# Kernel tuning notes

Measured on AMD Instinct MI355X. Metric: run time of the kernel, lower is better.

The kernel has to match this reference:

```python
import jax, jax.numpy as jnp
import numpy as np

NEG_SLOPE = 0.2  # PyG GATConv default negative_slope


def setup_inputs() -> dict:
    key = jax.random.key(0)
    k_x, k_e, k_w, k_as, k_ad = jax.random.split(key, 5)
    B, F, N, D, E, L = 2, 16, 5000, 128, 40000, 3
    x = jax.random.normal(k_x, (B, F, N, D), dtype=jnp.float32)
    edge_index = jax.random.randint(k_e, (B, F, 2, E), 0, N, dtype=jnp.int64)
    Ws = jax.random.normal(k_w, (L, D, D), dtype=jnp.float32) / np.float32(np.sqrt(D))
    att_src = jax.random.normal(k_as, (L, D), dtype=jnp.float32) / np.float32(np.sqrt(D))
    att_dst = jax.random.normal(k_ad, (L, D), dtype=jnp.float32) / np.float32(np.sqrt(D))
    bias = jnp.zeros((L, D), dtype=jnp.float32)
    return {"x": x, "edge_index": edge_index, "Ws": Ws,
            "att_src": att_src, "att_dst": att_dst, "bias": bias}


def _gat_layer(h, src, dst, n, W, a_s, a_d, b):
    # h: [n, D] node features; src/dst: [E_tot] edge endpoints (self-loops included)
    h2 = h @ W                                   # [n, D] transformed features
    s = h2 @ a_s                                 # [n] per-node source score
    d = h2 @ a_d                                 # [n] per-node dest score
    e = jax.nn.leaky_relu(s[src] + d[dst], NEG_SLOPE)   # [E_tot] raw attention
    m = jax.lax.stop_gradient(jax.ops.segment_max(e, dst, num_segments=n))
    ex = jnp.exp(e - m[dst])                     # numerically stable softmax per dst
    denom = jax.ops.segment_sum(ex, dst, num_segments=n)
    alpha = ex / denom[dst]                      # [E_tot] normalized attention
    out = jax.ops.segment_sum(alpha[:, None] * h2[src], dst, num_segments=n) + b
    return jax.nn.relu(out)


def reference(x, edge_index, Ws, att_src, att_dst, bias):
    B, F, N, D = x.shape
    n = B * F * N
    h = x.reshape(n, D)
    # faithful to torch: (BF,2,E).view(2,-1) is a raw row-major reshape
    ei = edge_index.reshape(2, -1)
    loop = jnp.arange(n, dtype=ei.dtype)         # PyG GATConv adds self-loops
    src = jnp.concatenate([ei[0], loop])
    dst = jnp.concatenate([ei[1], loop])
    for l in range(Ws.shape[0]):                 # fixed small layer loop
        h = _gat_layer(h, src, dst, n, Ws[l], att_src[l], att_dst[l], bias[l])
    return h.reshape(B, F, N, D)
```

## Files before the change

kernel.cpp:

```cpp
#include <hip/hip_runtime.h>
#include <math.h>

#define NODES_TOTAL 160000
#define NODES_REAL  5000
#define D 128
#define NEG 0.2f
#define KP2 128
#define HL2 (128 * KP2)
#define WT2_L (2 * HL2)
#define CHUNK 16384

typedef unsigned short ushort_t;
typedef unsigned int uint_t;
typedef __attribute__((ext_vector_type(8))) __bf16 bf16x8;
typedef __attribute__((ext_vector_type(4))) float f32x4;
union BF8 { bf16x8 v; ushort_t u[8]; };

__device__ __forceinline__ void split2(float x, ushort_t& hi, ushort_t& lo) {
    unsigned u = __float_as_uint(x);
    hi = (ushort_t)(u >> 16);
    float hif = __uint_as_float(u & 0xffff0000u);
    lo = (ushort_t)(__float_as_uint(x - hif) >> 16);
}
__device__ __forceinline__ uint_t encmax(float f) {
    uint_t b = __float_as_uint(f);
    return b ^ ((uint_t)((int)b >> 31) | 0x80000000u);
}
__device__ __forceinline__ float decmax(uint_t u) {
    uint_t b = (u & 0x80000000u) ? (u ^ 0x80000000u) : ~u;
    return __uint_as_float(b);
}

__global__ void wsplit_kernel(const float* __restrict__ Ws, ushort_t* __restrict__ Wm,
                              int* __restrict__ counts, uint_t* __restrict__ gmaxu) {
    int gid = blockIdx.x * 256 + threadIdx.x;
    if (gid < NODES_REAL) counts[gid] = 0;
    if (gid < 3) gmaxu[gid] = 0u;
    int l  = blockIdx.x >> 3;
    int n  = (blockIdx.x & 7) * 16 + (threadIdx.x >> 4);
    int c8 = threadIdx.x & 15;
    int k0 = c8 * 8;
    const float* src = Ws + (size_t)l * D * D;
    union { ushort_t u[8]; uint4 v; } hi, lo;
    #pragma unroll
    for (int j = 0; j < 8; ++j) split2(src[(size_t)(k0 + j) * D + n], hi.u[j], lo.u[j]);
    int ct = n >> 4, m16 = n & 15, kc = c8 >> 2, qq = c8 & 3;
    int lane = qq * 16 + m16;
    ushort_t* d2 = Wm + (size_t)l * WT2_L + ((ct * 4 + kc) * 2 + 0) * 512 + lane * 8;
    *(uint4*)d2 = hi.v;
    *(uint4*)(d2 + 512) = lo.v;
}

__global__ __launch_bounds__(256)
void rank2_kernel(const int* __restrict__ ei, int* __restrict__ counts,
                  int* __restrict__ bases, ushort_t* __restrict__ rank16, int Eh) {
    __shared__ uint_t lc[NODES_REAL];
    int c = blockIdx.x, tid = threadIdx.x;
    for (int i = tid; i < NODES_REAL; i += 256) lc[i] = 0u;
    __syncthreads();
    int e0 = c * CHUNK;
    #pragma unroll 4
    for (int k = 0; k < CHUNK / 256; ++k) {
        int e = e0 + k * 256 + tid;
        if (e < Eh) {
            int d = ei[Eh + e];
            uint_t r = atomicAdd(&lc[d], 1u);
            rank16[e] = (ushort_t)r;
        }
    }
    __syncthreads();
    for (int i = tid; i < NODES_REAL; i += 256) {
        uint_t n = lc[i];
        if (n > 0u)
            bases[c * NODES_REAL + i] = atomicAdd(&counts[i], (int)n);
    }
}

__global__ void scan_kernel(const int* __restrict__ counts, int* __restrict__ offs) {
    __shared__ int sd[1024];
    int t = threadIdx.x;
    int pre[5]; int sum = 0;
    #pragma unroll
    for (int u = 0; u < 5; ++u) {
        int idx = t * 5 + u;
        int c = (idx < NODES_REAL) ? counts[idx] : 0;
        pre[u] = sum; sum += c;
    }
    sd[t] = sum;
    __syncthreads();
    int run = sum;
    for (int o = 1; o < 1024; o <<= 1) {
        int v = (t >= o) ? sd[t - o] : 0;
        __syncthreads();
        sd[t] += v;
        __syncthreads();
    }
    int excl = sd[t] - run;
    #pragma unroll
    for (int u = 0; u < 5; ++u) {
        int idx = t * 5 + u;
        if (idx < NODES_REAL) offs[idx] = excl + pre[u];
    }
    if (t == 1023) offs[NODES_REAL] = excl + run;
}

__global__ void scatter_det(const int* __restrict__ ei, const int* __restrict__ offs,
                            const int* __restrict__ bases,
                            const ushort_t* __restrict__ rank16, ushort_t* __restrict__ esrc,
                            int Eh) {
    int e = blockIdx.x * blockDim.x + threadIdx.x;
    if (e < Eh) {
        int s = ei[e];
        int d = ei[Eh + e];
        int c = e >> 14;
        esrc[offs[d] + bases[c * NODES_REAL + d] + (int)rank16[e]] = (ushort_t)s;
    }
}

__global__ __launch_bounds__(256, 2)
void mlp3_kernel(const float* __restrict__ x, const ushort_t* __restrict__ Wm,
                 const float* __restrict__ bs, float* __restrict__ out) {
    __shared__ float scr[2][2][16][132];
    int tid = threadIdx.x;
    int w = tid >> 6, lane = tid & 63, q = lane >> 4, m16 = lane & 15;
    int p = w >> 1, h = w & 1;
    int row0 = NODES_REAL + blockIdx.x * 64 + p * 32;

    float4 xa[2][4][2];
    #pragma unroll
    for (int rt = 0; rt < 2; ++rt) {
        int r = row0 + rt * 16 + m16;
        if (r > NODES_TOTAL - 1) r = NODES_TOTAL - 1;
        #pragma unroll
        for (int kc = 0; kc < 4; ++kc) {
            const float* gp = x + (size_t)r * D + kc * 32 + q * 8;
            xa[rt][kc][0] = *(const float4*)gp;
            xa[rt][kc][1] = *(const float4*)(gp + 4);
        }
    }

    f32x4 acc[2][4];
    #pragma unroll
    for (int l = 0; l < 3; ++l) {
        const ushort_t* Wml = Wm + (size_t)l * WT2_L;
        if (l > 0) __syncthreads();

        BF8 ahi[2][4], alo[2][4];
        #pragma unroll
        for (int rt = 0; rt < 2; ++rt)
            #pragma unroll
            for (int kc = 0; kc < 4; ++kc) {
                float4 v0, v1;
                if (l == 0) { v0 = xa[rt][kc][0]; v1 = xa[rt][kc][1]; }
                else {
                    const float* sp = &scr[p][rt][m16][kc * 32 + q * 8];
                    v0 = *(const float4*)sp; v1 = *(const float4*)(sp + 4);
                }
                float xv[8] = {v0.x, v0.y, v0.z, v0.w, v1.x, v1.y, v1.z, v1.w};
                #pragma unroll
                for (int j = 0; j < 8; ++j) split2(xv[j], ahi[rt][kc].u[j], alo[rt][kc].u[j]);
            }
        if (l > 0) __syncthreads();

        #pragma unroll
        for (int rt = 0; rt < 2; ++rt)
            #pragma unroll
            for (int ct = 0; ct < 4; ++ct) acc[rt][ct] = (f32x4){0.f, 0.f, 0.f, 0.f};

        #pragma unroll
        for (int ph = 0; ph < 2; ++ph) {
            int kc0 = ph * 2;
            bf16x8 bh[4][2], bl[4][2];
            #pragma unroll
            for (int ct = 0; ct < 4; ++ct)
                #pragma unroll
                for (int dk = 0; dk < 2; ++dk) {
                    const ushort_t* bp = Wml + (((h * 4 + ct) * 4 + (kc0 + dk)) * 2) * 512 + lane * 8;
                    bh[ct][dk] = *(const bf16x8*)bp;
                    bl[ct][dk] = *(const bf16x8*)(bp + 512);
                }
            #pragma unroll
            for (int dk = 0; dk < 2; ++dk)
                #pragma unroll
                for (int ct = 0; ct < 4; ++ct)
                    #pragma unroll
                    for (int rt = 0; rt < 2; ++rt) {
                        acc[rt][ct] = __builtin_amdgcn_mfma_f32_16x16x32_bf16(ahi[rt][kc0 + dk].v, bh[ct][dk], acc[rt][ct], 0, 0, 0);
                        acc[rt][ct] = __builtin_amdgcn_mfma_f32_16x16x32_bf16(ahi[rt][kc0 + dk].v, bl[ct][dk], acc[rt][ct], 0, 0, 0);
                        acc[rt][ct] = __builtin_amdgcn_mfma_f32_16x16x32_bf16(alo[rt][kc0 + dk].v, bh[ct][dk], acc[rt][ct], 0, 0, 0);
                    }
        }
        float bv[4];
        #pragma unroll
        for (int ct = 0; ct < 4; ++ct) bv[ct] = bs[l * D + (h * 4 + ct) * 16 + m16];
        #pragma unroll
        for (int rt = 0; rt < 2; ++rt)
            #pragma unroll
            for (int ct = 0; ct < 4; ++ct)
                #pragma unroll
                for (int reg = 0; reg < 4; ++reg)
                    scr[p][rt][q * 4 + reg][(h * 4 + ct) * 16 + m16] =
                        fmaxf(acc[rt][ct][reg] + bv[ct], 0.f);
    }
    __syncthreads();
    #pragma unroll
    for (int i = 0; i < 8; ++i) {
        int rowl = i * 2 + (lane >> 5);
        int grow = row0 + h * 16 + rowl;
        float4 v = *(const float4*)&scr[p][h][rowl][(lane & 31) * 4];
        if (grow < NODES_TOTAL)
            *(float4*)&out[(size_t)grow * D + (lane & 31) * 4] = v;
    }
}

__global__ __launch_bounds__(64, 2)
void gsmall_kernel(const float* __restrict__ hin, const ushort_t* __restrict__ Wm,
                   const float* __restrict__ a_s, const float* __restrict__ a_d,
                   float* __restrict__ h2, float* __restrict__ sv, float* __restrict__ dv,
                   uint_t* __restrict__ gmaxu) {
    int lane = threadIdx.x & 63, q = lane >> 4, m16 = lane & 15;
    int row0 = blockIdx.x * 16;
    float4 xa[4][2];
    {
        int r = row0 + m16;
        if (r > NODES_REAL - 1) r = NODES_REAL - 1;
        #pragma unroll
        for (int kc = 0; kc < 4; ++kc) {
            const float* gp = hin + (size_t)r * D + kc * 32 + q * 8;
            xa[kc][0] = *(const float4*)gp;
            xa[kc][1] = *(const float4*)(gp + 4);
        }
    }
    f32x4 acc[8];
    #pragma unroll
    for (int ct = 0; ct < 8; ++ct) acc[ct] = (f32x4){0.f, 0.f, 0.f, 0.f};

    #pragma unroll
    for (int kc = 0; kc < 4; ++kc) {
        BF8 ahi, alo;
        {
            float4 v0 = xa[kc][0], v1 = xa[kc][1];
            float xv[8] = {v0.x, v0.y, v0.z, v0.w, v1.x, v1.y, v1.z, v1.w};
            #pragma unroll
            for (int j = 0; j < 8; ++j) split2(xv[j], ahi.u[j], alo.u[j]);
        }
        bf16x8 bh[8], bl[8];
        #pragma unroll
        for (int ct = 0; ct < 8; ++ct) {
            const ushort_t* bp = Wm + ((ct * 4 + kc) * 2) * 512 + lane * 8;
            bh[ct] = *(const bf16x8*)bp;
            bl[ct] = *(const bf16x8*)(bp + 512);
        }
        #pragma unroll
        for (int ct = 0; ct < 8; ++ct) {
            acc[ct] = __builtin_amdgcn_mfma_f32_16x16x32_bf16(ahi.v, bh[ct], acc[ct], 0, 0, 0);
            acc[ct] = __builtin_amdgcn_mfma_f32_16x16x32_bf16(ahi.v, bl[ct], acc[ct], 0, 0, 0);
            acc[ct] = __builtin_amdgcn_mfma_f32_16x16x32_bf16(alo.v, bh[ct], acc[ct], 0, 0, 0);
        }
    }
    #pragma unroll
    for (int reg = 0; reg < 4; ++reg) {
        int grow = row0 + q * 4 + reg;
        if (grow < NODES_REAL) {
            #pragma unroll
            for (int ct = 0; ct < 8; ++ct)
                h2[(size_t)grow * D + ct * 16 + m16] = acc[ct][reg];
        }
    }
    float asv[8], adv[8];
    #pragma unroll
    for (int ct = 0; ct < 8; ++ct) { asv[ct] = a_s[ct * 16 + m16]; adv[ct] = a_d[ct * 16 + m16]; }
    #pragma unroll
    for (int reg = 0; reg < 4; ++reg) {
        float ps = 0.f, pd = 0.f;
        #pragma unroll
        for (int ct = 0; ct < 8; ++ct) {
            float v = acc[ct][reg];
            ps += v * asv[ct]; pd += v * adv[ct];
        }
        #pragma unroll
        for (int o = 1; o < 16; o <<= 1) { ps += __shfl_xor(ps, o); pd += __shfl_xor(pd, o); }
        int grow = row0 + q * 4 + reg;
        if (m16 == 0 && grow < NODES_REAL) {
            sv[grow] = ps; dv[grow] = pd;
            atomicMax(gmaxu, encmax(ps));
        }
    }
}

__global__ __launch_bounds__(256)
void agg_kernel(const float* __restrict__ h2, const float* __restrict__ sv,
                const float* __restrict__ dv, const int* __restrict__ offs,
                const ushort_t* __restrict__ esrc, const float* __restrict__ bias,
                float* __restrict__ out, const uint_t* __restrict__ gmaxu) {
    int w = threadIdx.x >> 6, lane = threadIdx.x & 63;
    int i = blockIdx.x * 4 + w;
    int start = offs[i], end = offs[i + 1];
    float d_i = dv[i];
    float gm = decmax(*gmaxu) + d_i;
    float m = gm > 0.f ? gm : NEG * gm;
    const float2* h2v = (const float2*)h2;
    float ax0 = 0.f, ay0 = 0.f, ax1 = 0.f, ay1 = 0.f;
    float ax2 = 0.f, ay2 = 0.f, ax3 = 0.f, ay3 = 0.f, exs = 0.f;
    for (int base = start; base < end; base += 64) {
        int cnt = min(64, end - base);
        int srci = (lane < cnt) ? (int)esrc[base + lane] : 0;
        float sc = sv[srci] + d_i;
        sc = sc > 0.f ? sc : NEG * sc;
        float ex = (lane < cnt) ? __expf(sc - m) : 0.f;
        exs += ex;
        if (cnt == 64) {
            float e0 = __shfl(ex, 0), e1 = __shfl(ex, 1);
            float e2 = __shfl(ex, 2), e3 = __shfl(ex, 3);
            float2 hv0 = h2v[(size_t)__shfl(srci, 0) * 64 + lane];
            float2 hv1 = h2v[(size_t)__shfl(srci, 1) * 64 + lane];
            float2 hv2 = h2v[(size_t)__shfl(srci, 2) * 64 + lane];
            float2 hv3 = h2v[(size_t)__shfl(srci, 3) * 64 + lane];
            for (int j = 4; j < 64; j += 4) {
                float f0 = __shfl(ex, j),     f1 = __shfl(ex, j + 1);
                float f2 = __shfl(ex, j + 2), f3 = __shfl(ex, j + 3);
                float2 nv0 = h2v[(size_t)__shfl(srci, j) * 64 + lane];
                float2 nv1 = h2v[(size_t)__shfl(srci, j + 1) * 64 + lane];
                float2 nv2 = h2v[(size_t)__shfl(srci, j + 2) * 64 + lane];
                float2 nv3 = h2v[(size_t)__shfl(srci, j + 3) * 64 + lane];
                ax0 += e0 * hv0.x; ay0 += e0 * hv0.y;
                ax1 += e1 * hv1.x; ay1 += e1 * hv1.y;
                ax2 += e2 * hv2.x; ay2 += e2 * hv2.y;
                ax3 += e3 * hv3.x; ay3 += e3 * hv3.y;
                e0 = f0; e1 = f1; e2 = f2; e3 = f3;
                hv0 = nv0; hv1 = nv1; hv2 = nv2; hv3 = nv3;
            }
            ax0 += e0 * hv0.x; ay0 += e0 * hv0.y;
            ax1 += e1 * hv1.x; ay1 += e1 * hv1.y;
            ax2 += e2 * hv2.x; ay2 += e2 * hv2.y;
            ax3 += e3 * hv3.x; ay3 += e3 * hv3.y;
        } else {
            for (int j = 0; j < cnt; ++j) {
                int   src = __shfl(srci, j);
                float e   = __shfl(ex, j);
                float2 hv = h2v[(size_t)src * 64 + lane];
                ax0 += e * hv.x; ay0 += e * hv.y;
            }
        }
    }
    float ax = (ax0 + ax1) + (ax2 + ax3);
    float ay = (ay0 + ay1) + (ay2 + ay3);
    float scf = sv[i] + d_i; scf = scf > 0.f ? scf : NEG * scf;
    float exf = __expf(scf - m);
    float2 hv = h2v[(size_t)i * 64 + lane];
    ax += exf * hv.x; ay += exf * hv.y;
    #pragma unroll
    for (int o = 1; o < 64; o <<= 1) exs += __shfl_xor(exs, o);
    float rd = 1.f / (exs + exf);
    float2 b2 = *(const float2*)&bias[2 * lane];
    float2 o2 = make_float2(fmaxf(ax * rd + b2.x, 0.f), fmaxf(ay * rd + b2.y, 0.f));
    *(float2*)&out[(size_t)i * D + 2 * lane] = o2;
}

extern "C" void kernel_launch(void* const* d_in, const int* in_sizes, int n_in,
                              void* d_out, int out_size, void* d_ws, size_t ws_size,
                              hipStream_t stream) {
    const float* x   = (const float*)d_in[0];
    const int*   ei  = (const int*)d_in[1];
    const float* Ws  = (const float*)d_in[2];
    const float* as_ = (const float*)d_in[3];
    const float* ad_ = (const float*)d_in[4];
    const float* bs  = (const float*)d_in[5];
    float* out = (float*)d_out;
    int Eh = in_sizes[1] / 2;
    int nchunks = (Eh + CHUNK - 1) / CHUNK;

    char* ws = (char*)d_ws;
    float*    h2     = (float*)ws;
    float*    bufS   = (float*)(ws + 2560000);
    float*    sv     = (float*)(ws + 5120000);
    float*    dv     = (float*)(ws + 5140000);
    int*      counts = (int*)  (ws + 5160000);
    int*      offs   = (int*)  (ws + 5180000);
    ushort_t* rank16 = (ushort_t*)(ws + 5200016);
    ushort_t* esrc   = (ushort_t*)(ws + 7760016);
    ushort_t* Wm     = (ushort_t*)(ws + 10320016);
    uint_t*   gmaxu  = (uint_t*)(ws + 10528912);
    int*      bases  = (int*)h2;

    wsplit_kernel<<<24, 256, 0, stream>>>(Ws, Wm, counts, gmaxu);
    rank2_kernel<<<nchunks, 256, 0, stream>>>(ei, counts, bases, rank16, Eh);
    scan_kernel<<<1, 1024, 0, stream>>>(counts, offs);
    scatter_det<<<(Eh + 255) / 256, 256, 0, stream>>>(ei, offs, bases, rank16, esrc, Eh);

    mlp3_kernel<<<(NODES_TOTAL - NODES_REAL + 63) / 64, 256, 0, stream>>>(x, Wm, bs, out);

    for (int l = 0; l < 3; ++l) {
        const float* hin = (l == 0) ? x : bufS;
        float* hout = (l == 2) ? out : bufS;
        gsmall_kernel<<<(NODES_REAL + 15) / 16, 64, 0, stream>>>(
            hin, Wm + (size_t)l * WT2_L, as_ + l * D, ad_ + l * D, h2, sv, dv, gmaxu + l);
        agg_kernel<<<(NODES_REAL + 3) / 4, 256, 0, stream>>>(
            h2, sv, dv, offs, esrc, bs + l * D, hout, gmaxu + l);
    }
}
```

Measured before the change: 487.9 us.

## Split agg edges across four waves per node and split mlp3 launch

The aggregation kernel now gives one block of four waves to each destination node. Each wave takes a strided quarter of the edge list, and the partial sums are reduced through shared memory before wave 0 writes the output. The goal is more parallelism on the high-degree nodes, since all real nodes receive 16x more edges. The mlp3 kernel is also split into four sequential launches over row ranges, which adds launch overhead for no clear benefit.

```diff
diff --git a/kernel.cpp b/kernel.cpp
--- a/kernel.cpp
+++ b/kernel.cpp
@@ -119,12 +119,12 @@
 
 __global__ __launch_bounds__(256, 2)
 void mlp3_kernel(const float* __restrict__ x, const ushort_t* __restrict__ Wm,
-                 const float* __restrict__ bs, float* __restrict__ out) {
+                 const float* __restrict__ bs, float* __restrict__ out, int row_base) {
     __shared__ float scr[2][2][16][132];
     int tid = threadIdx.x;
     int w = tid >> 6, lane = tid & 63, q = lane >> 4, m16 = lane & 15;
     int p = w >> 1, h = w & 1;
-    int row0 = NODES_REAL + blockIdx.x * 64 + p * 32;
+    int row0 = row_base + blockIdx.x * 64 + p * 32;
 
     float4 xa[2][4][2];
     #pragma unroll
@@ -293,8 +293,10 @@
                 const float* __restrict__ dv, const int* __restrict__ offs,
                 const ushort_t* __restrict__ esrc, const float* __restrict__ bias,
                 float* __restrict__ out, const uint_t* __restrict__ gmaxu) {
+    __shared__ float2 red[4][64];
+    __shared__ float lexs[4];
     int w = threadIdx.x >> 6, lane = threadIdx.x & 63;
-    int i = blockIdx.x * 4 + w;
+    int i = blockIdx.x;
     int start = offs[i], end = offs[i + 1];
     float d_i = dv[i];
     float gm = decmax(*gmaxu) + d_i;
@@ -302,7 +304,7 @@
     const float2* h2v = (const float2*)h2;
     float ax0 = 0.f, ay0 = 0.f, ax1 = 0.f, ay1 = 0.f;
     float ax2 = 0.f, ay2 = 0.f, ax3 = 0.f, ay3 = 0.f, exs = 0.f;
-    for (int base = start; base < end; base += 64) {
+    for (int base = start + w * 64; base < end; base += 256) {
         int cnt = min(64, end - base);
         int srci = (lane < cnt) ? (int)esrc[base + lane] : 0;
         float sc = sv[srci] + d_i;
@@ -345,16 +347,25 @@
     }
     float ax = (ax0 + ax1) + (ax2 + ax3);
     float ay = (ay0 + ay1) + (ay2 + ay3);
-    float scf = sv[i] + d_i; scf = scf > 0.f ? scf : NEG * scf;
-    float exf = __expf(scf - m);
-    float2 hv = h2v[(size_t)i * 64 + lane];
-    ax += exf * hv.x; ay += exf * hv.y;
     #pragma unroll
     for (int o = 1; o < 64; o <<= 1) exs += __shfl_xor(exs, o);
-    float rd = 1.f / (exs + exf);
-    float2 b2 = *(const float2*)&bias[2 * lane];
-    float2 o2 = make_float2(fmaxf(ax * rd + b2.x, 0.f), fmaxf(ay * rd + b2.y, 0.f));
-    *(float2*)&out[(size_t)i * D + 2 * lane] = o2;
+    red[w][lane] = make_float2(ax, ay);
+    if (lane == 0) lexs[w] = exs;
+    __syncthreads();
+    if (w == 0) {
+        float2 r1 = red[1][lane], r2 = red[2][lane], r3 = red[3][lane];
+        ax += r1.x + r2.x + r3.x;
+        ay += r1.y + r2.y + r3.y;
+        float exst = lexs[0] + lexs[1] + lexs[2] + lexs[3];
+        float scf = sv[i] + d_i; scf = scf > 0.f ? scf : NEG * scf;
+        float exf = __expf(scf - m);
+        float2 hv = h2v[(size_t)i * 64 + lane];
+        ax += exf * hv.x; ay += exf * hv.y;
+        float rd = 1.f / (exst + exf);
+        float2 b2 = *(const float2*)&bias[2 * lane];
+        float2 o2 = make_float2(fmaxf(ax * rd + b2.x, 0.f), fmaxf(ay * rd + b2.y, 0.f));
+        *(float2*)&out[(size_t)i * D + 2 * lane] = o2;
+    }
 }
 
 extern "C" void kernel_launch(void* const* d_in, const int* in_sizes, int n_in,
@@ -388,14 +399,24 @@
     scan_kernel<<<1, 1024, 0, stream>>>(counts, offs);
     scatter_det<<<(Eh + 255) / 256, 256, 0, stream>>>(ei, offs, bases, rank16, esrc, Eh);
 
-    mlp3_kernel<<<(NODES_TOTAL - NODES_REAL + 63) / 64, 256, 0, stream>>>(x, Wm, bs, out);
+    {
+        const int rows = NODES_TOTAL - NODES_REAL;
+        const int nb   = (rows + 63) / 64;
+        const int nb1  = (nb + 3) / 4;
+        for (int s = 0; s < 4; ++s) {
+            int b0 = s * nb1;
+            int bn = (s == 3) ? (nb - 3 * nb1) : nb1;
+            if (bn <= 0) break;
+            mlp3_kernel<<<bn, 256, 0, stream>>>(x, Wm, bs, out, NODES_REAL + b0 * 64);
+        }
+    }
 
     for (int l = 0; l < 3; ++l) {
         const float* hin = (l == 0) ? x : bufS;
         float* hout = (l == 2) ? out : bufS;
         gsmall_kernel<<<(NODES_REAL + 15) / 16, 64, 0, stream>>>(
             hin, Wm + (size_t)l * WT2_L, as_ + l * D, ad_ + l * D, h2, sv, dv, gmaxu + l);
-        agg_kernel<<<(NODES_REAL + 3) / 4, 256, 0, stream>>>(
+        agg_kernel<<<NODES_REAL, 256, 0, stream>>>(
             h2, sv, dv, offs, esrc, bs + l * D, hout, gmaxu + l);
     }
 }
```

Result: slower. 514.1 us (+5.4%).
